# Performance work log

Hardware: AMD Instinct MI355X
Metric: run time of the kernel (lower is better)

Reference implementation:

```python
import jax, jax.numpy as jnp
import numpy as np

B, C, H, W = 4, 64, 64, 64


def setup_inputs() -> dict:
    key = jax.random.key(0)
    ks = jax.random.split(key, 9)
    s = 1.0 / np.sqrt(C)
    return {
        "x1": jax.random.normal(ks[0], (B, C, H, W), dtype=jnp.float32),
        "x2": jax.random.normal(ks[1], (B, C, H, W), dtype=jnp.float32),
        "wq": jax.random.normal(ks[2], (C, C), dtype=jnp.float32) * s,
        "bq": jax.random.normal(ks[3], (C,), dtype=jnp.float32) * 0.01,
        "wk": jax.random.normal(ks[4], (C, C), dtype=jnp.float32) * s,
        "bk": jax.random.normal(ks[5], (C,), dtype=jnp.float32) * 0.01,
        "wv": jax.random.normal(ks[6], (C, C), dtype=jnp.float32) * s,
        "bv": jax.random.normal(ks[7], (C,), dtype=jnp.float32) * 0.01,
        "gamma": jax.random.normal(ks[8], (1,), dtype=jnp.float32) * 0.1,
    }


def _conv1x1(x, w, b):
    # 1x1 conv == per-pixel GEMM: [B,C,H,W] x [Cout,Cin] -> [B,Cout,H,W]
    return jnp.einsum('bchw,oc->bohw', x, w) + b[None, :, None, None]


def reference(x1, x2, wq, bq, wk, bk, wv, bv, gamma):
    b, c, h, w = x1.shape
    n = h * w
    q = _conv1x1(x1, wq, bq).reshape(b, c, n)   # [B,C,N]
    k = _conv1x1(x2, wk, bk).reshape(b, c, n)   # [B,C,N]
    v = _conv1x1(x2, wv, bv).reshape(b, c, n)   # [B,C,N]
    # attention[b,i,j] = sum_c q[b,c,i] * k[b,c,j]  -> [B,N,N]
    attn = jnp.einsum('bci,bcj->bij', q, k)
    attn = jax.nn.softmax(attn, axis=-1)
    # out[b,c,i] = sum_j v[b,c,j] * attn[b,i,j]
    out = jnp.einsum('bcj,bij->bci', v, attn).reshape(b, c, h, w)
    return gamma[0] * out + x1
```

## Files before the change

### kernel.cpp

```cpp
#include <hip/hip_runtime.h>
#include <cstdint>
#include <cstddef>


typedef __bf16 bf16x2 __attribute__((ext_vector_type(2)));
typedef __bf16 bf16x4 __attribute__((ext_vector_type(4)));
typedef __bf16 bf16x8 __attribute__((ext_vector_type(8)));
typedef float  f32x4  __attribute__((ext_vector_type(4)));
typedef float  f32x16 __attribute__((ext_vector_type(16)));

constexpr int C = 64;
constexpr int N = 4096;
constexpr float LOG2E = 1.44269504088896340736f;

static __device__ __forceinline__ f32x4 mfma16(bf16x8 a, bf16x8 b, f32x4 c) {
    return __builtin_amdgcn_mfma_f32_16x16x32_bf16(a, b, c, 0, 0, 0);
}
static __device__ __forceinline__ f32x16 mfma32(bf16x8 a, bf16x8 b, f32x16 c) {
    return __builtin_amdgcn_mfma_f32_32x32x16_bf16(a, b, c, 0, 0, 0);
}
static __device__ __forceinline__ float fast_exp2(float x) {
#if __has_builtin(__builtin_amdgcn_exp2f)
    return __builtin_amdgcn_exp2f(x);
#else
    return exp2f(x);
#endif
}
static __device__ __forceinline__ uint32_t pack2(float a, float b) {
    union { uint32_t u; bf16x2 h; } w;
    w.h = bf16x2{(__bf16)a, (__bf16)b};
    return w.u;
}

__global__ __launch_bounds__(256) void qkv_kernel(
    const float* __restrict__ x1, const float* __restrict__ x2,
    const float* __restrict__ wq, const float* __restrict__ bq,
    const float* __restrict__ wk, const float* __restrict__ bk,
    const float* __restrict__ wv, const float* __restrict__ bv,
    __bf16* __restrict__ qo, __bf16* __restrict__ ko, __bf16* __restrict__ vo)
{
    __shared__ __bf16 wl[64][72];
    __shared__ __bf16 tout[64][72];

    const int bid  = blockIdx.x;
    const int kind = bid >> 8;
    const int pg   = bid & 255;
    const int b     = pg >> 6;
    const int nbase = (pg & 63) * 64;
    const int tid   = threadIdx.x;

    const float* wsel = kind == 0 ? wq : (kind == 1 ? wk : wv);
    const float* bsel = kind == 0 ? bq : (kind == 1 ? bk : bv);
    const float* xsel = kind == 0 ? x1 : x2;
    __bf16*      osel = kind == 0 ? qo : (kind == 1 ? ko : vo);

#pragma unroll
    for (int i = 0; i < 4; ++i) {
        int idx = i * 256 + tid;
        int row = idx >> 4, c4 = (idx & 15) * 4;
        float4 a = *(const float4*)(wsel + row * 64 + c4);
        bf16x4 h = {(__bf16)a.x, (__bf16)a.y, (__bf16)a.z, (__bf16)a.w};
        *(bf16x4*)&wl[row][c4] = h;
    }
    __syncthreads();

    const int wave = tid >> 6, lane = tid & 63;
    const int l = lane & 15, qd = lane >> 4;
    const int p = nbase + wave * 16 + l;

    const float* xb = xsel + (size_t)b * C * N + p;
    bf16x8 ax[2];
#pragma unroll
    for (int ks = 0; ks < 2; ++ks)
#pragma unroll
        for (int j = 0; j < 8; ++j)
            ax[ks][j] = (__bf16)xb[(size_t)(ks * 32 + qd * 8 + j) * N];

    if (kind < 2) {
        const float scale = kind == 0 ? LOG2E : 1.0f;
#pragma unroll
        for (int ot = 0; ot < 4; ++ot) {
            const float bb = bsel[ot * 16 + l];
            f32x4 acc = {bb, bb, bb, bb};
#pragma unroll
            for (int ks = 0; ks < 2; ++ks) {
                bf16x8 bw = *(const bf16x8*)&wl[ot * 16 + l][ks * 32 + qd * 8];
                acc = mfma16(ax[ks], bw, acc);
            }
#pragma unroll
            for (int r = 0; r < 4; ++r) {
                int px = wave * 16 + qd * 4 + r;
                tout[px][ot * 16 + l] = (__bf16)(acc[r] * scale);
            }
        }
        __syncthreads();

        const int tile = tid >> 7, t7 = tid & 127;
        const int kc = t7 >> 5, h2 = (t7 >> 4) & 1, ilp = (t7 & 15) * 2;
        const size_t tb = ((size_t)b * 128 + (nbase >> 5) + tile) * 2048;
        const size_t off = tb + kc * 512 + h2 * 256 + ilp * 8;
        bf16x8 ra = *(const bf16x8*)&tout[tile * 32 + ilp][kc * 16 + h2 * 8];
        bf16x8 rb = *(const bf16x8*)&tout[tile * 32 + ilp + 1][kc * 16 + h2 * 8];
        *(bf16x8*)&osel[off]     = ra;
        *(bf16x8*)&osel[off + 8] = rb;
    } else {
#pragma unroll
        for (int ct = 0; ct < 4; ++ct) {
            f32x4 acc;
#pragma unroll
            for (int r = 0; r < 4; ++r) acc[r] = bsel[ct * 16 + qd * 4 + r];
#pragma unroll
            for (int ks = 0; ks < 2; ++ks) {
                bf16x8 aw = *(const bf16x8*)&wl[ct * 16 + l][ks * 32 + qd * 8];
                acc = mfma16(aw, ax[ks], acc);
            }
            bf16x4 pk = {(__bf16)acc[0], (__bf16)acc[1], (__bf16)acc[2], (__bf16)acc[3]};
            *(bf16x4*)&tout[wave * 16 + l][ct * 16 + qd * 4] = pk;
        }
        __syncthreads();

        const int tile = tid >> 7, t7 = tid & 127;
        const int G = t7 >> 6, vh = (t7 >> 5) & 1, il = t7 & 31;
        const int pxb = tile * 32 + G * 16 + vh * 8;
        bf16x8 oA, oB;
#pragma unroll
        for (int e = 0; e < 8; ++e) {
            oA[e] = tout[pxb + e][il];
            oB[e] = tout[pxb + e][32 + il];
        }
        const size_t tb = ((size_t)b * 128 + (nbase >> 5) + tile) * 2048;
        const size_t off = tb + G * 1024 + vh * 512 + (size_t)il * 16;
        *(bf16x8*)&osel[off]     = oA;
        *(bf16x8*)&osel[off + 8] = oB;
    }
}

__global__ __launch_bounds__(512, 2) void attn_kernel(
    const __bf16* __restrict__ qg, const __bf16* __restrict__ kg,
    const __bf16* __restrict__ vg, const float* __restrict__ x1,
    const float* __restrict__ gamma, float* __restrict__ out)
{
    __shared__ float lds_acc[3][64][64];
    __shared__ float lds_l[8][64];

    const int bid = blockIdx.x;
    const int xcd = bid & 7;
    const int b   = xcd >> 1;
    const int rt  = ((bid >> 3) << 1) | (xcd & 1);
    const int ibase = rt * 64;

    const int tid  = threadIdx.x;
    const int wave = tid >> 6, lane = tid & 63;
    const int il = lane & 31, hi = lane >> 5;

    const __bf16* qt = qg + ((size_t)b * 128 + rt * 2) * 2048;
    const __bf16* kt = kg + (size_t)b * 128 * 2048 + (size_t)(wave * 16) * 2048;
    const __bf16* vt = vg + (size_t)b * 128 * 2048 + (size_t)(wave * 16) * 2048;

    bf16x8 bqf[2][4];
#pragma unroll
    for (int qs = 0; qs < 2; ++qs)
#pragma unroll
        for (int kc = 0; kc < 4; ++kc)
            bqf[qs][kc] = *(const bf16x8*)(qt + qs * 2048 + kc * 512 + lane * 8);

    f32x16 zf;
#pragma unroll
    for (int r = 0; r < 16; ++r) zf[r] = 0.f;

    f32x16 accO[4];
#pragma unroll
    for (int a = 0; a < 4; ++a)
#pragma unroll
        for (int r = 0; r < 16; ++r) accO[a][r] = 0.f;
    float lsum[2] = {0.f, 0.f};

    bf16x8 akf[2][4];
    bf16x8 avf[2][2][2];

#pragma unroll
    for (int kc = 0; kc < 4; ++kc)
        akf[0][kc] = *(const bf16x8*)(kt + kc * 512 + lane * 8);
#pragma unroll
    for (int ct = 0; ct < 2; ++ct)
#pragma unroll
        for (int G = 0; G < 2; ++G)
            avf[0][ct][G] = *(const bf16x8*)(vt + G * 1024 + hi * 512 + il * 16 + ct * 8);

#pragma unroll 2
    for (int t = 0; t < 16; ++t) {
        const int cur = t & 1;
        if (t < 15) {
            const size_t nb = (size_t)(t + 1) * 2048;
#pragma unroll
            for (int kc = 0; kc < 4; ++kc)
                akf[cur ^ 1][kc] = *(const bf16x8*)(kt + nb + kc * 512 + lane * 8);
#pragma unroll
            for (int ct = 0; ct < 2; ++ct)
#pragma unroll
                for (int G = 0; G < 2; ++G)
                    avf[cur ^ 1][ct][G] = *(const bf16x8*)(vt + nb + G * 1024 + hi * 512 + il * 16 + ct * 8);
        }

#pragma unroll
        for (int qs = 0; qs < 2; ++qs) {
            f32x16 st = mfma32(akf[cur][0], bqf[qs][0], zf);
#pragma unroll
            for (int kc = 1; kc < 4; ++kc) st = mfma32(akf[cur][kc], bqf[qs][kc], st);

            float e0, e1;
            float lp0 = 0.f, lp1 = 0.f;
            uint32_t a0, a1, b0, b1, c0, c1, d0, d1;
            e0 = fast_exp2(st[0]);  e1 = fast_exp2(st[1]);
            lp0 += e0; lp1 += e1; a0 = pack2(e0, e1);
            e0 = fast_exp2(st[2]);  e1 = fast_exp2(st[3]);
            lp0 += e0; lp1 += e1; a1 = pack2(e0, e1);
            e0 = fast_exp2(st[4]);  e1 = fast_exp2(st[5]);
            lp0 += e0; lp1 += e1; b0 = pack2(e0, e1);
            e0 = fast_exp2(st[6]);  e1 = fast_exp2(st[7]);
            lp0 += e0; lp1 += e1; b1 = pack2(e0, e1);
            e0 = fast_exp2(st[8]);  e1 = fast_exp2(st[9]);
            lp0 += e0; lp1 += e1; c0 = pack2(e0, e1);
            e0 = fast_exp2(st[10]); e1 = fast_exp2(st[11]);
            lp0 += e0; lp1 += e1; c1 = pack2(e0, e1);
            e0 = fast_exp2(st[12]); e1 = fast_exp2(st[13]);
            lp0 += e0; lp1 += e1; d0 = pack2(e0, e1);
            e0 = fast_exp2(st[14]); e1 = fast_exp2(st[15]);
            lp0 += e0; lp1 += e1; d1 = pack2(e0, e1);
            lsum[qs] += lp0 + lp1;

            asm("v_permlane32_swap_b32 %0, %1" : "+v"(a0), "+v"(b0));
            asm("v_permlane32_swap_b32 %0, %1" : "+v"(a1), "+v"(b1));
            asm("v_permlane32_swap_b32 %0, %1" : "+v"(c0), "+v"(d0));
            asm("v_permlane32_swap_b32 %0, %1" : "+v"(c1), "+v"(d1));
            union F { uint32_t u[4]; bf16x8 v; } f0, f1;
            f0.u[0] = a0; f0.u[1] = a1; f0.u[2] = b0; f0.u[3] = b1;
            f1.u[0] = c0; f1.u[1] = c1; f1.u[2] = d0; f1.u[3] = d1;

#pragma unroll
            for (int ct = 0; ct < 2; ++ct) {
                accO[qs * 2 + ct] = mfma32(avf[cur][ct][0], f0.v, accO[qs * 2 + ct]);
                accO[qs * 2 + ct] = mfma32(avf[cur][ct][1], f1.v, accO[qs * 2 + ct]);
            }
        }
    }

#pragma unroll
    for (int qs = 0; qs < 2; ++qs) lsum[qs] += __shfl_xor(lsum[qs], 32);
    if (hi == 0) {
        lds_l[wave][il]      = lsum[0];
        lds_l[wave][32 + il] = lsum[1];
    }

#define ACC_STORE(SLOT)                                                        \
    do {                                                                       \
        _Pragma("unroll")                                                      \
        for (int qs = 0; qs < 2; ++qs)                                         \
            _Pragma("unroll")                                                  \
            for (int ct = 0; ct < 2; ++ct)                                     \
                _Pragma("unroll")                                              \
                for (int r = 0; r < 16; ++r)                                   \
                    lds_acc[SLOT][ct * 32 + (r & 3) + 8 * (r >> 2) + 4 * hi][qs * 32 + il] = accO[qs * 2 + ct][r]; \
    } while (0)
#define ACC_LOAD(SLOT)                                                         \
    do {                                                                       \
        _Pragma("unroll")                                                      \
        for (int qs = 0; qs < 2; ++qs)                                         \
            _Pragma("unroll")                                                  \
            for (int ct = 0; ct < 2; ++ct)                                     \
                _Pragma("unroll")                                              \
                for (int r = 0; r < 16; ++r)                                   \
                    accO[qs * 2 + ct][r] += lds_acc[SLOT][ct * 32 + (r & 3) + 8 * (r >> 2) + 4 * hi][qs * 32 + il]; \
    } while (0)

    if (wave >= 5) ACC_STORE(wave - 5);
    __syncthreads();
    if (wave >= 1 && wave <= 3) ACC_LOAD(wave - 1);
    __syncthreads();
    if (wave >= 2 && wave <= 4) ACC_STORE(wave - 2);
    __syncthreads();
    if (wave <= 1) ACC_LOAD(wave);
    if (wave == 0) ACC_LOAD(2);
    __syncthreads();
    if (wave == 1) ACC_STORE(0);
    __syncthreads();
    if (wave == 0) { ACC_LOAD(0); ACC_STORE(0); }
    __syncthreads();
#undef ACC_STORE
#undef ACC_LOAD

    const float g = gamma[0];
    {
        const int c  = tid >> 3;
        const int i8 = (tid & 7) * 8;
        float lv[8];
#pragma unroll
        for (int e = 0; e < 8; ++e) {
            float s = 0.f;
#pragma unroll
            for (int w = 0; w < 8; ++w) s += lds_l[w][i8 + e];
            lv[e] = s;
        }
        const size_t idx = ((size_t)b * C + c) * N + ibase + i8;
        f32x4 o0 = *(const f32x4*)&lds_acc[0][c][i8];
        f32x4 o1 = *(const f32x4*)&lds_acc[0][c][i8 + 4];
        f32x4 x0 = *(const f32x4*)(x1 + idx);
        f32x4 x4 = *(const f32x4*)(x1 + idx + 4);
        f32x4 r0, r1;
#pragma unroll
        for (int e = 0; e < 4; ++e) {
            r0[e] = g * o0[e] / lv[e] + x0[e];
            r1[e] = g * o1[e] / lv[4 + e] + x4[e];
        }
        *(f32x4*)(out + idx) = r0;
        *(f32x4*)(out + idx + 4) = r1;
    }
}

extern "C" void kernel_launch(void* const* d_in, const int* in_sizes, int n_in,
                              void* d_out, int out_size, void* d_ws, size_t ws_size,
                              hipStream_t stream) {
    const float* x1    = (const float*)d_in[0];
    const float* x2    = (const float*)d_in[1];
    const float* wq    = (const float*)d_in[2];
    const float* bqv   = (const float*)d_in[3];
    const float* wk    = (const float*)d_in[4];
    const float* bkv   = (const float*)d_in[5];
    const float* wv    = (const float*)d_in[6];
    const float* bvv   = (const float*)d_in[7];
    const float* gamma = (const float*)d_in[8];
    float* out = (float*)d_out;

    __bf16* qws = (__bf16*)d_ws;
    __bf16* kws = qws + (size_t)4 * 128 * 2048;
    __bf16* vws = kws + (size_t)4 * 128 * 2048;

    qkv_kernel<<<768, 256, 0, stream>>>(x1, x2, wq, bqv, wk, bkv, wv, bvv, qws, kws, vws);
    attn_kernel<<<256, 512, 0, stream>>>(qws, kws, vws, x1, gamma, out);
}
```

Baseline: 99.34 us.

## Split attention channel tiles across wave pairs with 1024-thread blocks

The attention kernel doubles its block to 16 waves. Each pair of waves shares a key/value slice and splits the two 32-channel output tiles between them, so each wave holds half as many output accumulators. Both waves in a pair recompute the same QK scores and exponentials, which doubles that work. The explicit double-buffered prefetch of K/V fragments is dropped in favour of plain per-iteration loads. The larger launch bound may also constrain the register budget enough to cause spills, in exchange for more waves to hide latency.

```diff
diff --git a/kernel.cpp b/kernel.cpp
--- a/kernel.cpp
+++ b/kernel.cpp
@@ -135,7 +135,7 @@
     }
 }
 
-__global__ __launch_bounds__(512, 2) void attn_kernel(
+__global__ __launch_bounds__(1024, 4) void attn_kernel(
     const __bf16* __restrict__ qg, const __bf16* __restrict__ kg,
     const __bf16* __restrict__ vg, const float* __restrict__ x1,
     const float* __restrict__ gamma, float* __restrict__ out)
@@ -151,11 +151,12 @@
 
     const int tid  = threadIdx.x;
     const int wave = tid >> 6, lane = tid & 63;
+    const int jg = wave >> 1, ctw = wave & 1;
     const int il = lane & 31, hi = lane >> 5;
 
     const __bf16* qt = qg + ((size_t)b * 128 + rt * 2) * 2048;
-    const __bf16* kt = kg + (size_t)b * 128 * 2048 + (size_t)(wave * 16) * 2048;
-    const __bf16* vt = vg + (size_t)b * 128 * 2048 + (size_t)(wave * 16) * 2048;
+    const __bf16* kt = kg + (size_t)b * 128 * 2048 + (size_t)(jg * 16) * 2048;
+    const __bf16* vt = vg + (size_t)b * 128 * 2048 + (size_t)(jg * 16) * 2048;
 
     bf16x8 bqf[2][4];
 #pragma unroll
@@ -164,49 +165,31 @@
         for (int kc = 0; kc < 4; ++kc)
             bqf[qs][kc] = *(const bf16x8*)(qt + qs * 2048 + kc * 512 + lane * 8);
 
-    f32x16 zf;
-#pragma unroll
-    for (int r = 0; r < 16; ++r) zf[r] = 0.f;
-
-    f32x16 accO[4];
-#pragma unroll
-    for (int a = 0; a < 4; ++a)
+    f32x16 accO[2];
+#pragma unroll
+    for (int a = 0; a < 2; ++a)
 #pragma unroll
         for (int r = 0; r < 16; ++r) accO[a][r] = 0.f;
     float lsum[2] = {0.f, 0.f};
 
-    bf16x8 akf[2][4];
-    bf16x8 avf[2][2][2];
-
-#pragma unroll
-    for (int kc = 0; kc < 4; ++kc)
-        akf[0][kc] = *(const bf16x8*)(kt + kc * 512 + lane * 8);
-#pragma unroll
-    for (int ct = 0; ct < 2; ++ct)
-#pragma unroll
-        for (int G = 0; G < 2; ++G)
-            avf[0][ct][G] = *(const bf16x8*)(vt + G * 1024 + hi * 512 + il * 16 + ct * 8);
-
 #pragma unroll 2
     for (int t = 0; t < 16; ++t) {
-        const int cur = t & 1;
-        if (t < 15) {
-            const size_t nb = (size_t)(t + 1) * 2048;
-#pragma unroll
-            for (int kc = 0; kc < 4; ++kc)
-                akf[cur ^ 1][kc] = *(const bf16x8*)(kt + nb + kc * 512 + lane * 8);
-#pragma unroll
-            for (int ct = 0; ct < 2; ++ct)
-#pragma unroll
-                for (int G = 0; G < 2; ++G)
-                    avf[cur ^ 1][ct][G] = *(const bf16x8*)(vt + nb + G * 1024 + hi * 512 + il * 16 + ct * 8);
-        }
+        const size_t tb = (size_t)t * 2048;
+        bf16x8 ak[4], av[2];
+#pragma unroll
+        for (int kc = 0; kc < 4; ++kc)
+            ak[kc] = *(const bf16x8*)(kt + tb + kc * 512 + lane * 8);
+#pragma unroll
+        for (int G = 0; G < 2; ++G)
+            av[G] = *(const bf16x8*)(vt + tb + G * 1024 + hi * 512 + il * 16 + ctw * 8);
 
 #pragma unroll
         for (int qs = 0; qs < 2; ++qs) {
-            f32x16 st = mfma32(akf[cur][0], bqf[qs][0], zf);
-#pragma unroll
-            for (int kc = 1; kc < 4; ++kc) st = mfma32(akf[cur][kc], bqf[qs][kc], st);
+            f32x16 st;
+#pragma unroll
+            for (int r = 0; r < 16; ++r) st[r] = 0.f;
+#pragma unroll
+            for (int kc = 0; kc < 4; ++kc) st = mfma32(ak[kc], bqf[qs][kc], st);
 
             float e0, e1;
             float lp0 = 0.f, lp1 = 0.f;
@@ -237,19 +220,16 @@
             f0.u[0] = a0; f0.u[1] = a1; f0.u[2] = b0; f0.u[3] = b1;
             f1.u[0] = c0; f1.u[1] = c1; f1.u[2] = d0; f1.u[3] = d1;
 
-#pragma unroll
-            for (int ct = 0; ct < 2; ++ct) {
-                accO[qs * 2 + ct] = mfma32(avf[cur][ct][0], f0.v, accO[qs * 2 + ct]);
-                accO[qs * 2 + ct] = mfma32(avf[cur][ct][1], f1.v, accO[qs * 2 + ct]);
-            }
+            accO[qs] = mfma32(av[0], f0.v, accO[qs]);
+            accO[qs] = mfma32(av[1], f1.v, accO[qs]);
         }
     }
 
 #pragma unroll
     for (int qs = 0; qs < 2; ++qs) lsum[qs] += __shfl_xor(lsum[qs], 32);
-    if (hi == 0) {
-        lds_l[wave][il]      = lsum[0];
-        lds_l[wave][32 + il] = lsum[1];
+    if (ctw == 0 && hi == 0) {
+        lds_l[jg][il]      = lsum[0];
+        lds_l[jg][32 + il] = lsum[1];
     }
 
 #define ACC_STORE(SLOT)                                                        \
@@ -257,63 +237,53 @@
         _Pragma("unroll")                                                      \
         for (int qs = 0; qs < 2; ++qs)                                         \
             _Pragma("unroll")                                                  \
-            for (int ct = 0; ct < 2; ++ct)                                     \
-                _Pragma("unroll")                                              \
-                for (int r = 0; r < 16; ++r)                                   \
-                    lds_acc[SLOT][ct * 32 + (r & 3) + 8 * (r >> 2) + 4 * hi][qs * 32 + il] = accO[qs * 2 + ct][r]; \
+            for (int r = 0; r < 16; ++r)                                       \
+                lds_acc[SLOT][ctw * 32 + (r & 3) + 8 * (r >> 2) + 4 * hi][qs * 32 + il] = accO[qs][r]; \
     } while (0)
 #define ACC_LOAD(SLOT)                                                         \
     do {                                                                       \
         _Pragma("unroll")                                                      \
         for (int qs = 0; qs < 2; ++qs)                                         \
             _Pragma("unroll")                                                  \
-            for (int ct = 0; ct < 2; ++ct)                                     \
-                _Pragma("unroll")                                              \
-                for (int r = 0; r < 16; ++r)                                   \
-                    accO[qs * 2 + ct][r] += lds_acc[SLOT][ct * 32 + (r & 3) + 8 * (r >> 2) + 4 * hi][qs * 32 + il]; \
+            for (int r = 0; r < 16; ++r)                                       \
+                accO[qs][r] += lds_acc[SLOT][ctw * 32 + (r & 3) + 8 * (r >> 2) + 4 * hi][qs * 32 + il]; \
     } while (0)
 
-    if (wave >= 5) ACC_STORE(wave - 5);
-    __syncthreads();
-    if (wave >= 1 && wave <= 3) ACC_LOAD(wave - 1);
-    __syncthreads();
-    if (wave >= 2 && wave <= 4) ACC_STORE(wave - 2);
-    __syncthreads();
-    if (wave <= 1) ACC_LOAD(wave);
-    if (wave == 0) ACC_LOAD(2);
-    __syncthreads();
-    if (wave == 1) ACC_STORE(0);
-    __syncthreads();
-    if (wave == 0) { ACC_LOAD(0); ACC_STORE(0); }
+    if (jg >= 5) ACC_STORE(jg - 5);
+    __syncthreads();
+    if (jg >= 1 && jg <= 3) ACC_LOAD(jg - 1);
+    __syncthreads();
+    if (jg >= 2 && jg <= 4) ACC_STORE(jg - 2);
+    __syncthreads();
+    if (jg <= 1) ACC_LOAD(jg);
+    if (jg == 0) ACC_LOAD(2);
+    __syncthreads();
+    if (jg == 1) ACC_STORE(0);
+    __syncthreads();
+    if (jg == 0) { ACC_LOAD(0); ACC_STORE(0); }
     __syncthreads();
 #undef ACC_STORE
 #undef ACC_LOAD
 
     const float g = gamma[0];
     {
-        const int c  = tid >> 3;
-        const int i8 = (tid & 7) * 8;
-        float lv[8];
-#pragma unroll
-        for (int e = 0; e < 8; ++e) {
-            float s = 0.f;
-#pragma unroll
-            for (int w = 0; w < 8; ++w) s += lds_l[w][i8 + e];
-            lv[e] = s;
-        }
-        const size_t idx = ((size_t)b * C + c) * N + ibase + i8;
-        f32x4 o0 = *(const f32x4*)&lds_acc[0][c][i8];
-        f32x4 o1 = *(const f32x4*)&lds_acc[0][c][i8 + 4];
+        const int c  = tid >> 4;
+        const int i4 = (tid & 15) * 4;
+        f32x4 lv = {0.f, 0.f, 0.f, 0.f};
+#pragma unroll
+        for (int w = 0; w < 8; ++w) {
+            f32x4 lw = *(const f32x4*)&lds_l[w][i4];
+#pragma unroll
+            for (int e = 0; e < 4; ++e) lv[e] += lw[e];
+        }
+        const size_t idx = ((size_t)b * C + c) * N + ibase + i4;
+        f32x4 o0 = *(const f32x4*)&lds_acc[0][c][i4];
         f32x4 x0 = *(const f32x4*)(x1 + idx);
-        f32x4 x4 = *(const f32x4*)(x1 + idx + 4);
-        f32x4 r0, r1;
-#pragma unroll
-        for (int e = 0; e < 4; ++e) {
+        f32x4 r0;
+#pragma unroll
+        for (int e = 0; e < 4; ++e)
             r0[e] = g * o0[e] / lv[e] + x0[e];
-            r1[e] = g * o1[e] / lv[4 + e] + x4[e];
-        }
         *(f32x4*)(out + idx) = r0;
-        *(f32x4*)(out + idx + 4) = r1;
     }
 }
 
@@ -336,5 +306,5 @@
     __bf16* vws = kws + (size_t)4 * 128 * 2048;
 
     qkv_kernel<<<768, 256, 0, stream>>>(x1, x2, wq, bqv, wk, bkv, wv, bvv, qws, kws, vws);
-    attn_kernel<<<256, 512, 0, stream>>>(qws, kws, vws, x1, gamma, out);
-}
+    attn_kernel<<<256, 1024, 0, stream>>>(qws, kws, vws, x1, gamma, out);
+}
```

Result: slower. 141.2 us (+42.1%).
